# Kernel tuning notes

Hardware: AMD Instinct MI355X
Metric: run time of the kernel (lower is better)

Reference implementation:

```python
import jax, jax.numpy as jnp
import numpy as np

B, N, T = 1, 1024, 2048   # batch, graph nodes, timesteps
E, K = 16384, 32          # edges, causal kernel taps


def setup_inputs() -> dict:
    key = jax.random.key(0)
    k1, k2, k3, k4 = jax.random.split(key, 4)
    x = jax.random.normal(k1, (B, N, T), dtype=jnp.float32)
    # per-edge causal impulse-response kernels (aggregator(g) output)
    kernel = jax.random.normal(k2, (E, K), dtype=jnp.float32) * 0.1
    src = jax.random.randint(k3, (E,), 0, N)
    dst = jax.random.randint(k4, (E,), 0, N)
    return {"x": x, "kernel": kernel, "src": src, "dst": dst}


def reference(x, kernel, src, dst):
    # Block-sparse causal conv over the edge list:
    #   y_e[b, t] = sum_k kernel[e, k] * x[b, src_e, t - k]   (causal)
    #   out[b, n, t] = x[b, n, t] + sum_{e: dst_e = n} y_e[b, t]
    # (residual applied because g.include_index_diag is False)
    xs = x[:, src, :]                      # [B, E, T] gather upstream signals
    rhs = kernel[:, None, ::-1]            # [E, 1, K] flipped -> true causal conv
    y = jax.lax.conv_general_dilated(
        xs, rhs,
        window_strides=(1,),
        padding=[(K - 1, 0)],              # left-pad: strictly causal
        dimension_numbers=("NCW", "OIW", "NCW"),
        feature_group_count=E,             # one independent kernel per edge
    )                                      # [B, E, T]
    agg = jax.ops.segment_sum(jnp.swapaxes(y, 0, 1), dst, num_segments=N)  # [N, B, T]
    return x + jnp.swapaxes(agg, 0, 1)     # [B, N, T]
```

## Files before the change

kernel.cpp:

```cpp
#include <hip/hip_runtime.h>
#include <hip/hip_bf16.h>

#define TT  2048
#define KK  32
#define NN  1024
#define EE  16384
#define CAP 64

typedef short short8 __attribute__((ext_vector_type(8)));
typedef float f32x4 __attribute__((ext_vector_type(4)));

__device__ __forceinline__ short f2bf(float f) {
    __hip_bfloat16 h = __float2bfloat16(f);
    return __builtin_bit_cast(short, h);
}

__global__ __launch_bounds__(256, 4) void lti_kernel(
    const float* __restrict__ x,
    const float* __restrict__ kern,
    const int*   __restrict__ src,
    const int*   __restrict__ dst,
    float*       __restrict__ out)
{
    const int n   = blockIdx.x;
    const int tid = threadIdx.x;
    const int w   = tid >> 6;
    const int ln  = tid & 63;
    const int c   = ln & 15, g = ln >> 4;
    const int t0  = 512 * w;

    __shared__ __align__(16) short xs_all[4][544];
    __shared__ __align__(16) short kt_all[4][8][72];
    __shared__ int bl[CAP];
    __shared__ int bc;

    short* xs = xs_all[w];
    short (*kt)[72] = kt_all[w];

    short8 z8; z8[0]=0;z8[1]=0;z8[2]=0;z8[3]=0;z8[4]=0;z8[5]=0;z8[6]=0;z8[7]=0;

    if (tid == 0) bc = 0;
    {
        short8* kz = (short8*)&kt[0][0];
        kz[ln] = z8;
        if (ln < 8) kz[64 + ln] = z8;
        if (w == 0 && ln < 4) *(short8*)&xs[8 * ln] = z8;
    }
    __syncthreads();

    const int4* d4 = (const int4*)dst;
    #pragma unroll
    for (int it = 0; it < EE / 1024; ++it) {
        const int i4 = tid + 256 * it;
        const int4 d = d4[i4];
        const int eb = 4 * i4;
        if (d.x == n) { int p = atomicAdd(&bc, 1); if (p < CAP) bl[p] = (src[eb    ] << 14) | (eb    ); }
        if (d.y == n) { int p = atomicAdd(&bc, 1); if (p < CAP) bl[p] = (src[eb + 1] << 14) | (eb + 1); }
        if (d.z == n) { int p = atomicAdd(&bc, 1); if (p < CAP) bl[p] = (src[eb + 2] << 14) | (eb + 2); }
        if (d.w == n) { int p = atomicAdd(&bc, 1); if (p < CAP) bl[p] = (src[eb + 3] << 14) | (eb + 3); }
    }
    __syncthreads();
    int L = bc; if (L > CAP) L = CAP;

    f32x4 acc0 = {0,0,0,0}, acc1 = {0,0,0,0};
    short8 rowA, rowB, haloA = z8, haloB = z8;
    float4 tapA = {0,0,0,0}, tapB = {0,0,0,0};

    #define LOAD_EX(S, SV)                                                             \
    {                                                                                  \
        const int e0 = __builtin_amdgcn_readfirstlane((int)((SV) & 16383u));           \
        const int s0 = __builtin_amdgcn_readfirstlane((int)((SV) >> 14));              \
        const float4* xr = (const float4*)(x + (size_t)s0 * TT + t0);                  \
        float4 u = xr[2 * ln], v = xr[2 * ln + 1];                                     \
        row##S[0]=f2bf(u.x); row##S[1]=f2bf(u.y); row##S[2]=f2bf(u.z); row##S[3]=f2bf(u.w); \
        row##S[4]=f2bf(v.x); row##S[5]=f2bf(v.y); row##S[6]=f2bf(v.z); row##S[7]=f2bf(v.w); \
        if (w && ln < 4) {                                                             \
            u = *(const float4*)(x + (size_t)s0 * TT + t0 - 32 + 8 * ln);              \
            v = *(const float4*)(x + (size_t)s0 * TT + t0 - 28 + 8 * ln);              \
            halo##S[0]=f2bf(u.x); halo##S[1]=f2bf(u.y); halo##S[2]=f2bf(u.z); halo##S[3]=f2bf(u.w); \
            halo##S[4]=f2bf(v.x); halo##S[5]=f2bf(v.y); halo##S[6]=f2bf(v.z); halo##S[7]=f2bf(v.w); \
        }                                                                              \
        tap##S = *(const float4*)(kern + (size_t)e0 * KK + 4 * (ln & 7));              \
    }

    #define COMMIT_EX(S)                                                               \
    {                                                                                  \
        *(short8*)&xs[32 + 8 * ln] = row##S;                                           \
        if (w && ln < 4) *(short8*)&xs[8 * ln] = halo##S;                              \
        {        \
            const int a2  = ln >> 3;                                                   \
            const int pad = (a2 + 1) & 7;                                              \
            const int mb  = 4 * (ln & 7);                                              \
            kt[a2][pad + 47 - mb]     = f2bf(tap##S.x);                                \
            kt[a2][pad + 46 - mb]     = f2bf(tap##S.y);                                \
            kt[a2][pad + 45 - mb]     = f2bf(tap##S.z);                                \
            kt[a2][pad + 44 - mb]     = f2bf(tap##S.w);                                \
        }                                                                              \
    }

    const int a_ = c & 7;
    const int s1 = ((a_ + 1) & 7) + 15 - c + 8 * g;

    #define COMPUTE()                                                                  \
    {                                                                                  \
        const short8 b1 = *(const short8*)&kt[a_][s1];                                 \
        short8 b2 = *(const short8*)&kt[a_][s1 + 16];                                  \
        if (g < 2) b2 = z8;                              \
        {                                                                              \
            const short8 a1  = *(const short8*)&xs[16 * c + 8 * g];                    \
            const short8 a2v = *(const short8*)&xs[16 * c + 8 * g + 16];               \
            acc0 = __builtin_amdgcn_mfma_f32_16x16x32_bf16(a1,  b1, acc0, 0, 0, 0);    \
            acc0 = __builtin_amdgcn_mfma_f32_16x16x32_bf16(a2v, b2, acc0, 0, 0, 0);    \
        }                                                                              \
        {                                                                              \
            const short8 a1  = *(const short8*)&xs[256 + 16 * c + 8 * g];              \
            const short8 a2v = *(const short8*)&xs[256 + 16 * c + 8 * g + 16];         \
            acc1 = __builtin_amdgcn_mfma_f32_16x16x32_bf16(a1,  b1, acc1, 0, 0, 0);    \
            acc1 = __builtin_amdgcn_mfma_f32_16x16x32_bf16(a2v, b2, acc1, 0, 0, 0);    \
        }                                                                              \
    }

    if (L > 0) {
        unsigned svA = (unsigned)bl[0];
        LOAD_EX(A, svA);
        COMMIT_EX(A);
        if (L > 1) { unsigned svB = (unsigned)bl[1]; LOAD_EX(B, svB); }
        svA = (L > 2) ? (unsigned)bl[2] : 0u;

        for (int p = 0; p < L; p += 2) {
            const unsigned svC = (p + 3 < L) ? (unsigned)bl[p + 3] : 0u;
            COMPUTE();
            if (p + 2 < L) LOAD_EX(A, svA);
            if (p + 1 < L) { COMMIT_EX(B); COMPUTE(); }
            if (p + 4 < L) svA = (unsigned)bl[p + 4];
            if (p + 3 < L) LOAD_EX(B, svC);
            if (p + 2 < L) COMMIT_EX(A);
        }
    }

    const float* xr  = x   + (size_t)n * TT + t0;
    float*       orw = out + (size_t)n * TT + t0;
    #pragma unroll
    for (int q = 0; q < 4; ++q) {
        const int ta = 64 * g + 16 * q + c;
        orw[ta]       = xr[ta]       + acc0[q];
        orw[256 + ta] = xr[256 + ta] + acc1[q];
    }
    #undef LOAD_EX
    #undef COMMIT_EX
    #undef COMPUTE
}

extern "C" void kernel_launch(void* const* d_in, const int* in_sizes, int n_in,
                              void* d_out, int out_size, void* d_ws, size_t ws_size,
                              hipStream_t stream) {
    const float* x    = (const float*)d_in[0];
    const float* kern = (const float*)d_in[1];
    const int*   src  = (const int*)d_in[2];
    const int*   dst  = (const int*)d_in[3];
    float*       out  = (float*)d_out;

    lti_kernel<<<dim3(NN), dim3(256), 0, stream>>>(x, kern, src, dst, out);
}
```

Before: 42.90 us.

## Split each node's edge list across two wave groups with LDS reduction

Doubles the block to 512 threads so two groups of four waves each process alternating edges of the node's incoming edge list, halving the serial per-wave edge loop. The second group writes its partial accumulators to a new shared reduction buffer, and the first group adds them before the residual store. The dst scan is also split over twice as many threads. In exchange it adds LDS usage, an extra barrier, and more registers per block, which may reduce occupancy.

```diff
diff --git a/kernel.cpp b/kernel.cpp
--- a/kernel.cpp
+++ b/kernel.cpp
@@ -15,7 +15,7 @@
     return __builtin_bit_cast(short, h);
 }
 
-__global__ __launch_bounds__(256, 4) void lti_kernel(
+__global__ __launch_bounds__(512, 8) void lti_kernel(
     const float* __restrict__ x,
     const float* __restrict__ kern,
     const int*   __restrict__ src,
@@ -24,18 +24,21 @@
 {
     const int n   = blockIdx.x;
     const int tid = threadIdx.x;
-    const int w   = tid >> 6;
+    const int v   = tid >> 6;
+    const int w   = v & 3;
+    const int q   = v >> 2;
     const int ln  = tid & 63;
     const int c   = ln & 15, g = ln >> 4;
     const int t0  = 512 * w;
 
-    __shared__ __align__(16) short xs_all[4][544];
-    __shared__ __align__(16) short kt_all[4][8][72];
+    __shared__ __align__(16) short xs_all[8][544];
+    __shared__ __align__(16) short kt_all[8][8][72];
+    __shared__ __align__(16) float red[4][512];
     __shared__ int bl[CAP];
     __shared__ int bc;
 
-    short* xs = xs_all[w];
-    short (*kt)[72] = kt_all[w];
+    short* xs = xs_all[v];
+    short (*kt)[72] = kt_all[v];
 
     short8 z8; z8[0]=0;z8[1]=0;z8[2]=0;z8[3]=0;z8[4]=0;z8[5]=0;z8[6]=0;z8[7]=0;
 
@@ -50,8 +53,8 @@
 
     const int4* d4 = (const int4*)dst;
     #pragma unroll
-    for (int it = 0; it < EE / 1024; ++it) {
-        const int i4 = tid + 256 * it;
+    for (int it = 0; it < EE / 2048; ++it) {
+        const int i4 = tid + 512 * it;
         const int4 d = d4[i4];
         const int eb = 4 * i4;
         if (d.x == n) { int p = atomicAdd(&bc, 1); if (p < CAP) bl[p] = (src[eb    ] << 14) | (eb    ); }
@@ -61,6 +64,8 @@
     }
     __syncthreads();
     int L = bc; if (L > CAP) L = CAP;
+    const int M = (L - q + 1) >> 1;
+    #define IDX(I) (q + 2 * (I))
 
     f32x4 acc0 = {0,0,0,0}, acc1 = {0,0,0,0};
     short8 rowA, rowB, haloA = z8, haloB = z8;
@@ -71,14 +76,14 @@
         const int e0 = __builtin_amdgcn_readfirstlane((int)((SV) & 16383u));           \
         const int s0 = __builtin_amdgcn_readfirstlane((int)((SV) >> 14));              \
         const float4* xr = (const float4*)(x + (size_t)s0 * TT + t0);                  \
-        float4 u = xr[2 * ln], v = xr[2 * ln + 1];                                     \
+        float4 u = xr[2 * ln], vv = xr[2 * ln + 1];                                    \
         row##S[0]=f2bf(u.x); row##S[1]=f2bf(u.y); row##S[2]=f2bf(u.z); row##S[3]=f2bf(u.w); \
-        row##S[4]=f2bf(v.x); row##S[5]=f2bf(v.y); row##S[6]=f2bf(v.z); row##S[7]=f2bf(v.w); \
+        row##S[4]=f2bf(vv.x); row##S[5]=f2bf(vv.y); row##S[6]=f2bf(vv.z); row##S[7]=f2bf(vv.w); \
         if (w && ln < 4) {                                                             \
-            u = *(const float4*)(x + (size_t)s0 * TT + t0 - 32 + 8 * ln);              \
-            v = *(const float4*)(x + (size_t)s0 * TT + t0 - 28 + 8 * ln);              \
+            u  = *(const float4*)(x + (size_t)s0 * TT + t0 - 32 + 8 * ln);             \
+            vv = *(const float4*)(x + (size_t)s0 * TT + t0 - 28 + 8 * ln);             \
             halo##S[0]=f2bf(u.x); halo##S[1]=f2bf(u.y); halo##S[2]=f2bf(u.z); halo##S[3]=f2bf(u.w); \
-            halo##S[4]=f2bf(v.x); halo##S[5]=f2bf(v.y); halo##S[6]=f2bf(v.z); halo##S[7]=f2bf(v.w); \
+            halo##S[4]=f2bf(vv.x); halo##S[5]=f2bf(vv.y); halo##S[6]=f2bf(vv.z); halo##S[7]=f2bf(vv.w); \
         }                                                                              \
         tap##S = *(const float4*)(kern + (size_t)e0 * KK + 4 * (ln & 7));              \
     }
@@ -87,14 +92,14 @@
     {                                                                                  \
         *(short8*)&xs[32 + 8 * ln] = row##S;                                           \
         if (w && ln < 4) *(short8*)&xs[8 * ln] = halo##S;                              \
-        {        \
+        {                  \
             const int a2  = ln >> 3;                                                   \
             const int pad = (a2 + 1) & 7;                                              \
             const int mb  = 4 * (ln & 7);                                              \
-            kt[a2][pad + 47 - mb]     = f2bf(tap##S.x);                                \
-            kt[a2][pad + 46 - mb]     = f2bf(tap##S.y);                                \
-            kt[a2][pad + 45 - mb]     = f2bf(tap##S.z);                                \
-            kt[a2][pad + 44 - mb]     = f2bf(tap##S.w);                                \
+            kt[a2][pad + 47 - mb] = f2bf(tap##S.x);                                    \
+            kt[a2][pad + 46 - mb] = f2bf(tap##S.y);                                    \
+            kt[a2][pad + 45 - mb] = f2bf(tap##S.z);                                    \
+            kt[a2][pad + 44 - mb] = f2bf(tap##S.w);                                    \
         }                                                                              \
     }
 
@@ -120,32 +125,46 @@
         }                                                                              \
     }
 
-    if (L > 0) {
-        unsigned svA = (unsigned)bl[0];
+    if (M > 0) {
+        unsigned svA = (unsigned)bl[IDX(0)];
         LOAD_EX(A, svA);
         COMMIT_EX(A);
-        if (L > 1) { unsigned svB = (unsigned)bl[1]; LOAD_EX(B, svB); }
-        svA = (L > 2) ? (unsigned)bl[2] : 0u;
+        if (M > 1) { unsigned svB = (unsigned)bl[IDX(1)]; LOAD_EX(B, svB); }
+        svA = (M > 2) ? (unsigned)bl[IDX(2)] : 0u;
 
-        for (int p = 0; p < L; p += 2) {
-            const unsigned svC = (p + 3 < L) ? (unsigned)bl[p + 3] : 0u;
+        for (int i = 0; i < M; i += 2) {
+            const unsigned svC = (i + 3 < M) ? (unsigned)bl[IDX(i + 3)] : 0u;
             COMPUTE();
-            if (p + 2 < L) LOAD_EX(A, svA);
-            if (p + 1 < L) { COMMIT_EX(B); COMPUTE(); }
-            if (p + 4 < L) svA = (unsigned)bl[p + 4];
-            if (p + 3 < L) LOAD_EX(B, svC);
-            if (p + 2 < L) COMMIT_EX(A);
+            if (i + 2 < M) LOAD_EX(A, svA);
+            if (i + 1 < M) { COMMIT_EX(B); COMPUTE(); }
+            if (i + 4 < M) svA = (unsigned)bl[IDX(i + 4)];
+            if (i + 3 < M) LOAD_EX(B, svC);
+            if (i + 2 < M) COMMIT_EX(A);
         }
     }
 
-    const float* xr  = x   + (size_t)n * TT + t0;
-    float*       orw = out + (size_t)n * TT + t0;
-    #pragma unroll
-    for (int q = 0; q < 4; ++q) {
-        const int ta = 64 * g + 16 * q + c;
-        orw[ta]       = xr[ta]       + acc0[q];
-        orw[256 + ta] = xr[256 + ta] + acc1[q];
+    if (q == 1) {
+        float* rd = &red[w][0];
+        #pragma unroll
+        for (int qd = 0; qd < 4; ++qd) {
+            const int ta = 64 * g + 16 * qd + c;
+            rd[ta]       = acc0[qd];
+            rd[256 + ta] = acc1[qd];
+        }
     }
+    __syncthreads();
+    if (q == 0) {
+        const float* rd  = &red[w][0];
+        const float* xr  = x   + (size_t)n * TT + t0;
+        float*       orw = out + (size_t)n * TT + t0;
+        #pragma unroll
+        for (int qd = 0; qd < 4; ++qd) {
+            const int ta = 64 * g + 16 * qd + c;
+            orw[ta]       = xr[ta]       + acc0[qd] + rd[ta];
+            orw[256 + ta] = xr[256 + ta] + acc1[qd] + rd[256 + ta];
+        }
+    }
+    #undef IDX
     #undef LOAD_EX
     #undef COMMIT_EX
     #undef COMPUTE
@@ -160,5 +179,5 @@
     const int*   dst  = (const int*)d_in[3];
     float*       out  = (float*)d_out;
 
-    lti_kernel<<<dim3(NN), dim3(256), 0, stream>>>(x, kern, src, dst, out);
+    lti_kernel<<<dim3(NN), dim3(512), 0, stream>>>(x, kern, src, dst, out);
 }
```

Result: faster. 41.05 us (-4.3%).

## Pre-convert inputs to bf16 and triple-buffer direct global-to-LDS loads

Applied to the files above, without the earlier changes.

Adds a prep kernel that converts x and the edge kernels to bf16 in global scratch buffers. The main kernel then streams source rows straight into LDS with global_load_lds through a three-stage buffer and explicit vmcnt waits, so each edge's load overlaps with MFMA compute on earlier edges. This halves the bytes moved per gathered row and removes the per-edge conversion from the hot loop. The cost is an extra launch and a full pass over x and the kernels, plus more LDS use while the launch bound is raised to 8 blocks per CU.

```diff
diff --git a/kernel.cpp b/kernel.cpp
--- a/kernel.cpp
+++ b/kernel.cpp
@@ -7,17 +7,48 @@
 #define EE  16384
 #define CAP 64
 
-typedef short short8 __attribute__((ext_vector_type(8)));
-typedef float f32x4 __attribute__((ext_vector_type(4)));
+typedef short short8  __attribute__((ext_vector_type(8)));
+typedef short short4v __attribute__((ext_vector_type(4)));
+typedef float f32x4   __attribute__((ext_vector_type(4)));
+
+__device__ short g_xbf[NN * TT];
+__device__ short g_kbf[EE * KK];
 
 __device__ __forceinline__ short f2bf(float f) {
     __hip_bfloat16 h = __float2bfloat16(f);
     return __builtin_bit_cast(short, h);
 }
 
-__global__ __launch_bounds__(256, 4) void lti_kernel(
+__device__ __forceinline__ void gload_lds16(const short* g, short* l) {
+    __builtin_amdgcn_global_load_lds(
+        (const __attribute__((address_space(1))) void*)(const void*)(g),
+        (__attribute__((address_space(3))) void*)(void*)(l), 16, 0, 0);
+}
+
+__global__ __launch_bounds__(256) void prep_kernel(const float* __restrict__ x,
+                                                   const float* __restrict__ kern) {
+    const int bid = blockIdx.x;
+    if (bid < NN) {
+        const int i = bid * 256 + threadIdx.x;
+        const float4* x4 = (const float4*)x;
+        const float4 a = x4[2 * i], b = x4[2 * i + 1];
+        short8 h;
+        h[0]=f2bf(a.x); h[1]=f2bf(a.y); h[2]=f2bf(a.z); h[3]=f2bf(a.w);
+        h[4]=f2bf(b.x); h[5]=f2bf(b.y); h[6]=f2bf(b.z); h[7]=f2bf(b.w);
+        ((short8*)g_xbf)[i] = h;
+    } else {
+        const int i = (bid - NN) * 256 + threadIdx.x;
+        const float4* k4 = (const float4*)kern;
+        const float4 a = k4[2 * i], b = k4[2 * i + 1];
+        short8 h;
+        h[0]=f2bf(a.x); h[1]=f2bf(a.y); h[2]=f2bf(a.z); h[3]=f2bf(a.w);
+        h[4]=f2bf(b.x); h[5]=f2bf(b.y); h[6]=f2bf(b.z); h[7]=f2bf(b.w);
+        ((short8*)g_kbf)[i] = h;
+    }
+}
+
+__global__ __launch_bounds__(256, 8) void lti_kernel(
     const float* __restrict__ x,
-    const float* __restrict__ kern,
     const int*   __restrict__ src,
     const int*   __restrict__ dst,
     float*       __restrict__ out)
@@ -28,14 +59,15 @@
     const int ln  = tid & 63;
     const int c   = ln & 15, g = ln >> 4;
     const int t0  = 512 * w;
+    const int hoff = w ? (t0 - 32) : 0;
 
-    __shared__ __align__(16) short xs_all[4][544];
+    __shared__ __align__(16) short xs_all[4][3][544];
     __shared__ __align__(16) short kt_all[4][8][72];
     __shared__ int bl[CAP];
     __shared__ int bc;
 
-    short* xs = xs_all[w];
-    short (*kt)[72] = kt_all[w];
+    short (*xsb)[544] = xs_all[w];
+    short (*kt)[72]   = kt_all[w];
 
     short8 z8; z8[0]=0;z8[1]=0;z8[2]=0;z8[3]=0;z8[4]=0;z8[5]=0;z8[6]=0;z8[7]=0;
 
@@ -44,7 +76,7 @@
         short8* kz = (short8*)&kt[0][0];
         kz[ln] = z8;
         if (ln < 8) kz[64 + ln] = z8;
-        if (w == 0 && ln < 4) *(short8*)&xs[8 * ln] = z8;
+        if (w == 0 && ln < 12) *(short8*)&xs_all[0][ln >> 2][8 * (ln & 3)] = z8;
     }
     __syncthreads();
 
@@ -63,92 +95,85 @@
     int L = bc; if (L > CAP) L = CAP;
 
     f32x4 acc0 = {0,0,0,0}, acc1 = {0,0,0,0};
-    short8 rowA, rowB, haloA = z8, haloB = z8;
-    float4 tapA = {0,0,0,0}, tapB = {0,0,0,0};
-
-    #define LOAD_EX(S, SV)                                                             \
-    {                                                                                  \
-        const int e0 = __builtin_amdgcn_readfirstlane((int)((SV) & 16383u));           \
-        const int s0 = __builtin_amdgcn_readfirstlane((int)((SV) >> 14));              \
-        const float4* xr = (const float4*)(x + (size_t)s0 * TT + t0);                  \
-        float4 u = xr[2 * ln], v = xr[2 * ln + 1];                                     \
-        row##S[0]=f2bf(u.x); row##S[1]=f2bf(u.y); row##S[2]=f2bf(u.z); row##S[3]=f2bf(u.w); \
-        row##S[4]=f2bf(v.x); row##S[5]=f2bf(v.y); row##S[6]=f2bf(v.z); row##S[7]=f2bf(v.w); \
-        if (w && ln < 4) {                                                             \
-            u = *(const float4*)(x + (size_t)s0 * TT + t0 - 32 + 8 * ln);              \
-            v = *(const float4*)(x + (size_t)s0 * TT + t0 - 28 + 8 * ln);              \
-            halo##S[0]=f2bf(u.x); halo##S[1]=f2bf(u.y); halo##S[2]=f2bf(u.z); halo##S[3]=f2bf(u.w); \
-            halo##S[4]=f2bf(v.x); halo##S[5]=f2bf(v.y); halo##S[6]=f2bf(v.z); halo##S[7]=f2bf(v.w); \
-        }                                                                              \
-        tap##S = *(const float4*)(kern + (size_t)e0 * KK + 4 * (ln & 7));              \
-    }
-
-    #define COMMIT_EX(S)                                                               \
-    {                                                                                  \
-        *(short8*)&xs[32 + 8 * ln] = row##S;                                           \
-        if (w && ln < 4) *(short8*)&xs[8 * ln] = halo##S;                              \
-        {        \
-            const int a2  = ln >> 3;                                                   \
-            const int pad = (a2 + 1) & 7;                                              \
-            const int mb  = 4 * (ln & 7);                                              \
-            kt[a2][pad + 47 - mb]     = f2bf(tap##S.x);                                \
-            kt[a2][pad + 46 - mb]     = f2bf(tap##S.y);                                \
-            kt[a2][pad + 45 - mb]     = f2bf(tap##S.z);                                \
-            kt[a2][pad + 44 - mb]     = f2bf(tap##S.w);                                \
-        }                                                                              \
-    }
+    short8  hr0, hr1, hr2;
+    short4v tr0, tr1, tr2;
 
     const int a_ = c & 7;
     const int s1 = ((a_ + 1) & 7) + 15 - c + 8 * g;
 
-    #define COMPUTE()                                                                  \
+    #define ISSUE(S, P)                                                                \
+    {                                                                                  \
+        const unsigned sv = (unsigned)bl[P];                                           \
+        const int e0 = __builtin_amdgcn_readfirstlane((int)(sv & 16383u));             \
+        const int s0 = __builtin_amdgcn_readfirstlane((int)(sv >> 14));                \
+        const short* rb = g_xbf + (size_t)s0 * TT;                                     \
+        gload_lds16(rb + t0 + 8 * ln, &xsb[S][32]);                                    \
+        if (ln < 4) hr##S = *(const short8*)(rb + hoff + 8 * ln);                      \
+        tr##S = *(const short4v*)(g_kbf + ((size_t)e0 << 5) + 4 * (ln & 7));           \
+    }
+
+    #define COMMIT(S)                                                                  \
+    {                                                                                  \
+        if (w && ln < 4) *(short8*)&xsb[S][8 * ln] = hr##S;                            \
+        const int a2 = ln >> 3, pad = (a2 + 1) & 7, mb = 4 * (ln & 7);                 \
+        kt[a2][pad + 47 - mb] = tr##S[0];                                              \
+        kt[a2][pad + 46 - mb] = tr##S[1];                                              \
+        kt[a2][pad + 45 - mb] = tr##S[2];                                              \
+        kt[a2][pad + 44 - mb] = tr##S[3];                                              \
+    }
+
+    #define COMPUTE(S)                                                                 \
     {                                                                                  \
         const short8 b1 = *(const short8*)&kt[a_][s1];                                 \
         short8 b2 = *(const short8*)&kt[a_][s1 + 16];                                  \
         if (g < 2) b2 = z8;                              \
         {                                                                              \
-            const short8 a1  = *(const short8*)&xs[16 * c + 8 * g];                    \
-            const short8 a2v = *(const short8*)&xs[16 * c + 8 * g + 16];               \
+            const short8 a1  = *(const short8*)&xsb[S][16 * c + 8 * g];                \
+            const short8 a2v = *(const short8*)&xsb[S][16 * c + 8 * g + 16];           \
             acc0 = __builtin_amdgcn_mfma_f32_16x16x32_bf16(a1,  b1, acc0, 0, 0, 0);    \
             acc0 = __builtin_amdgcn_mfma_f32_16x16x32_bf16(a2v, b2, acc0, 0, 0, 0);    \
         }                                                                              \
         {                                                                              \
-            const short8 a1  = *(const short8*)&xs[256 + 16 * c + 8 * g];              \
-            const short8 a2v = *(const short8*)&xs[256 + 16 * c + 8 * g + 16];         \
+            const short8 a1  = *(const short8*)&xsb[S][256 + 16 * c + 8 * g];          \
+            const short8 a2v = *(const short8*)&xsb[S][256 + 16 * c + 8 * g + 16];     \
             acc1 = __builtin_amdgcn_mfma_f32_16x16x32_bf16(a1,  b1, acc1, 0, 0, 0);    \
             acc1 = __builtin_amdgcn_mfma_f32_16x16x32_bf16(a2v, b2, acc1, 0, 0, 0);    \
         }                                                                              \
     }
 
-    if (L > 0) {
-        unsigned svA = (unsigned)bl[0];
-        LOAD_EX(A, svA);
-        COMMIT_EX(A);
-        if (L > 1) { unsigned svB = (unsigned)bl[1]; LOAD_EX(B, svB); }
-        svA = (L > 2) ? (unsigned)bl[2] : 0u;
+    #define BODY(SC, SN, I)                                                            \
+    if ((I) < L) {                                                                     \
+        __builtin_amdgcn_sched_barrier(0);                                             \
+        if ((I) + 2 < L) ISSUE(SN, (I) + 2);                                           \
+        const int rem = L - (I);                                                       \
+        if (rem >= 3)      { asm volatile("s_waitcnt vmcnt(6)" ::: "memory"); }        \
+        else if (rem == 2) { asm volatile("s_waitcnt vmcnt(3)" ::: "memory"); }        \
+        else               { asm volatile("s_waitcnt vmcnt(0)" ::: "memory"); }        \
+        __builtin_amdgcn_sched_barrier(0);                                             \
+        COMMIT(SC);                                                                    \
+        COMPUTE(SC);                                                                   \
+    }
 
-        for (int p = 0; p < L; p += 2) {
-            const unsigned svC = (p + 3 < L) ? (unsigned)bl[p + 3] : 0u;
-            COMPUTE();
-            if (p + 2 < L) LOAD_EX(A, svA);
-            if (p + 1 < L) { COMMIT_EX(B); COMPUTE(); }
-            if (p + 4 < L) svA = (unsigned)bl[p + 4];
-            if (p + 3 < L) LOAD_EX(B, svC);
-            if (p + 2 < L) COMMIT_EX(A);
-        }
+    if (L > 0) ISSUE(0, 0);
+    if (L > 1) ISSUE(1, 1);
+    for (int i = 0; i < L; i += 3) {
+        BODY(0, 2, i);
+        BODY(1, 0, i + 1);
+        BODY(2, 1, i + 2);
     }
 
     const float* xr  = x   + (size_t)n * TT + t0;
     float*       orw = out + (size_t)n * TT + t0;
     #pragma unroll
-    for (int q = 0; q < 4; ++q) {
-        const int ta = 64 * g + 16 * q + c;
-        orw[ta]       = xr[ta]       + acc0[q];
-        orw[256 + ta] = xr[256 + ta] + acc1[q];
+    for (int qd = 0; qd < 4; ++qd) {
+        const int ta = 64 * g + 16 * qd + c;
+        orw[ta]       = xr[ta]       + acc0[qd];
+        orw[256 + ta] = xr[256 + ta] + acc1[qd];
     }
-    #undef LOAD_EX
-    #undef COMMIT_EX
+    #undef ISSUE
+    #undef COMMIT
     #undef COMPUTE
+    #undef BODY
 }
 
 extern "C" void kernel_launch(void* const* d_in, const int* in_sizes, int n_in,
@@ -160,5 +185,6 @@
     const int*   dst  = (const int*)d_in[3];
     float*       out  = (float*)d_out;
 
-    lti_kernel<<<dim3(NN), dim3(256), 0, stream>>>(x, kern, src, dst, out);
+    prep_kernel<<<dim3(NN + EE * KK / 8 / 256), dim3(256), 0, stream>>>(x, kern);
+    lti_kernel<<<dim3(NN), dim3(256), 0, stream>>>(x, src, dst, out);
 }
```

After: 45.46 us. +6.0%, slower.
